# Kernel optimization log

Hardware: AMD Instinct MI355X
Metric: run time of the kernel (lower is better)

Reference implementation:

```python
import jax, jax.numpy as jnp
import numpy as np

DIM = 1024
CTX_DIM = 1024
VALUE_DIM = 1024
HEADS = 16
HEAD_DIM = DIM // HEADS        # q/k head dim = 64
V_HEAD_DIM = VALUE_DIM // HEADS
LN_EPS = 1e-5


def setup_inputs() -> dict:
    key = jax.random.key(0)
    k0, k1, k2, k3, k4 = jax.random.split(key, 5)
    B, N, M = 4, 1024, 1024
    x = jax.random.normal(k0, (B, N, DIM), jnp.float32)
    context = jax.random.normal(k1, (B, M, CTX_DIM), jnp.float32)
    # Linear weights stored as [in, out] (y = x @ W), matching torch Linear math
    Wq = jax.random.normal(k2, (DIM, DIM), jnp.float32) * (DIM ** -0.5)
    Wkv = jax.random.normal(k3, (CTX_DIM, DIM + VALUE_DIM), jnp.float32) * (CTX_DIM ** -0.5)
    Wt = jax.random.normal(k4, (HEADS, HEADS), jnp.float32) * (HEADS ** -0.5)
    gamma = jnp.ones((HEADS,), jnp.float32)
    beta = jnp.zeros((HEADS,), jnp.float32)
    return {"x": x, "context": context, "Wq": Wq, "Wkv": Wkv,
            "Wt": Wt, "gamma": gamma, "beta": beta}


def reference(x, context, Wq, Wkv, Wt, gamma, beta):
    B, N, _ = x.shape
    M = context.shape[1]
    # projections
    q = (x @ Wq).reshape(B, N, HEADS, HEAD_DIM).transpose(0, 2, 1, 3)       # [B,H,N,d]
    kv = context @ Wkv                                                      # [B,M,dim+vdim]
    k = kv[..., :DIM].reshape(B, M, HEADS, HEAD_DIM).transpose(0, 2, 1, 3)  # [B,H,M,d]
    v = kv[..., DIM:].reshape(B, M, HEADS, V_HEAD_DIM).transpose(0, 2, 1, 3)
    # scaled dot-product scores, fully materialized as in the original
    scale = HEAD_DIM ** -0.5
    dots = jnp.einsum('bhid,bhjd->bhij', q * scale, k)                      # [B,H,N,M]
    w = jax.nn.softmax(dots, axis=-1)
    # talking heads: Linear(heads,heads,bias=False) then LayerNorm(heads) over head axis
    w = jnp.einsum('bhij,hg->bgij', w, Wt)
    mu = jnp.mean(w, axis=1, keepdims=True)
    var = jnp.var(w, axis=1, keepdims=True)
    w = (w - mu) * jax.lax.rsqrt(var + LN_EPS)
    w = w * gamma[None, :, None, None] + beta[None, :, None, None]
    attn = jnp.einsum('bhij,bhjd->bhid', w, v)                              # [B,H,N,vd]
    out = attn.transpose(0, 2, 1, 3).reshape(B, N, VALUE_DIM)
    return out
```

## Files before the change

kernel.cpp:

```cpp
#include <hip/hip_runtime.h>
#include <hip/hip_bf16.h>

typedef __bf16 bf16;
typedef bf16 bf16x2 __attribute__((ext_vector_type(2)));
typedef bf16 bf16x4 __attribute__((ext_vector_type(4)));
typedef bf16 bf16x8 __attribute__((ext_vector_type(8)));
typedef float floatx4 __attribute__((ext_vector_type(4)));

#define MFMA_BF16(a, b, c) __builtin_amdgcn_mfma_f32_16x16x32_bf16((a), (b), (c), 0, 0, 0)

__global__ __launch_bounds__(256) void cvt_kernel(const float* __restrict__ in,
                                                  bf16* __restrict__ out, int n8) {
    int idx = blockIdx.x * 256 + threadIdx.x;
    if (idx >= n8) return;
    const float* src = in + (size_t)idx * 8;
    float4 f0 = *(const float4*)src;
    float4 f1 = *(const float4*)(src + 4);
    bf16x8 v = {(bf16)f0.x, (bf16)f0.y, (bf16)f0.z, (bf16)f0.w,
                (bf16)f1.x, (bf16)f1.y, (bf16)f1.z, (bf16)f1.w};
    *(bf16x8*)(out + (size_t)idx * 8) = v;
}

__global__ __launch_bounds__(256) void trans_kernel(const float* __restrict__ in,
                                                    bf16* __restrict__ out, int R, int C) {
    __shared__ float tile[32][33];
    const int t = threadIdx.x;
    const int r0 = blockIdx.y * 32, c0 = blockIdx.x * 32;
    int r = t >> 3, c4 = (t & 7) * 4;
    float4 v = *(const float4*)&in[(size_t)(r0 + r) * C + c0 + c4];
    tile[r][c4 + 0] = v.x; tile[r][c4 + 1] = v.y;
    tile[r][c4 + 2] = v.z; tile[r][c4 + 3] = v.w;
    __syncthreads();
    int rp = t >> 3, cp = (t & 7) * 4;
    bf16x4 w = {(bf16)tile[cp + 0][rp], (bf16)tile[cp + 1][rp],
                (bf16)tile[cp + 2][rp], (bf16)tile[cp + 3][rp]};
    *(bf16x4*)&out[(size_t)(c0 + rp) * R + r0 + cp] = w;
}

__global__ __launch_bounds__(256) void vtrans_kernel(const bf16* __restrict__ in,
                                                     bf16* __restrict__ out) {
    __shared__ bf16 tile[32][36];
    const int t = threadIdx.x;
    const int r0 = blockIdx.y * 32, c0 = blockIdx.x * 32;
    int r = t >> 3, c4 = (t & 7) * 4;
    bf16x4 v = *(const bf16x4*)&in[(size_t)(r0 + r) * 1024 + c0 + c4];
    tile[r][c4 + 0] = v[0]; tile[r][c4 + 1] = v[1];
    tile[r][c4 + 2] = v[2]; tile[r][c4 + 3] = v[3];
    __syncthreads();
    int rp = t >> 3, cp = (t & 7) * 4;
    int hd = c0 + rp;
    int b = r0 >> 10, j = (r0 & 1023) + cp;
    bf16x4 w = {tile[cp + 0][rp], tile[cp + 1][rp], tile[cp + 2][rp], tile[cp + 3][rp]};
    *(bf16x4*)&out[(size_t)(b * 1024 + hd) * 1024 + j] = w;
}

__global__ __launch_bounds__(256) void prep_wt_kernel(const float* __restrict__ Wt,
                                                      bf16* __restrict__ WtcT) {
    const int t = threadIdx.x;
    const int g = t >> 4, k = t & 15;
    float s = 0.f;
#pragma unroll
    for (int gg = 0; gg < 16; ++gg) s += Wt[k * 16 + gg];
    WtcT[g * 32 + k] = (bf16)(Wt[k * 16 + g] - s * 0.0625f);
    WtcT[g * 32 + 16 + k] = (bf16)0.f;
}

template <int MODE>
__global__ __launch_bounds__(256) void gemm128(const bf16* __restrict__ A,
                                               const bf16* __restrict__ B,
                                               bf16* __restrict__ C,
                                               bf16* __restrict__ V, int N) {
    __shared__ bf16 As[128 * 40];
    __shared__ bf16 Bs[128 * 40];
    const int t = threadIdx.x;
    const int wv = t >> 6, lane = t & 63, quad = lane >> 4, l15 = lane & 15;
    const int wr = wv >> 1, wc = wv & 1;
    const int m0 = blockIdx.y * 128, n0 = blockIdx.x * 128;
    const int ra = t >> 1, kc = (t & 1) * 16;

    floatx4 acc[4][4] = {};

    for (int k0 = 0; k0 < 1024; k0 += 32) {
        bf16x8 a0 = *(const bf16x8*)&A[(size_t)(m0 + ra) * 1024 + k0 + kc];
        bf16x8 a1 = *(const bf16x8*)&A[(size_t)(m0 + ra) * 1024 + k0 + kc + 8];
        bf16x8 b0 = *(const bf16x8*)&B[(size_t)(n0 + ra) * 1024 + k0 + kc];
        bf16x8 b1 = *(const bf16x8*)&B[(size_t)(n0 + ra) * 1024 + k0 + kc + 8];
        __syncthreads();
        *(bf16x8*)&As[ra * 40 + kc] = a0;
        *(bf16x8*)&As[ra * 40 + kc + 8] = a1;
        *(bf16x8*)&Bs[ra * 40 + kc] = b0;
        *(bf16x8*)&Bs[ra * 40 + kc + 8] = b1;
        __syncthreads();
        bf16x8 af[4], bfr[4];
#pragma unroll
        for (int mt = 0; mt < 4; ++mt)
            af[mt] = *(bf16x8*)&As[(wr * 64 + mt * 16 + l15) * 40 + quad * 8];
#pragma unroll
        for (int nt = 0; nt < 4; ++nt)
            bfr[nt] = *(bf16x8*)&Bs[(wc * 64 + nt * 16 + l15) * 40 + quad * 8];
#pragma unroll
        for (int mt = 0; mt < 4; ++mt)
#pragma unroll
            for (int nt = 0; nt < 4; ++nt)
                acc[mt][nt] = MFMA_BF16(af[mt], bfr[nt], acc[mt][nt]);
    }
#pragma unroll
    for (int mt = 0; mt < 4; ++mt)
#pragma unroll
        for (int nt = 0; nt < 4; ++nt)
#pragma unroll
            for (int r = 0; r < 4; ++r) {
                int m = m0 + wr * 64 + mt * 16 + quad * 4 + r;
                int n = n0 + wc * 64 + nt * 16 + l15;
                bf16 val = (bf16)acc[mt][nt][r];
                if (MODE == 0) {
                    C[(size_t)m * N + n] = val;
                } else {
                    if (n < 1024) C[(size_t)m * 1024 + n] = val;
                    else          V[(size_t)m * 1024 + (n - 1024)] = val;
                }
            }
}

__global__ __launch_bounds__(256, 4) void denom_kernel(const bf16* __restrict__ Qb,
                                                       const bf16* __restrict__ Kb,
                                                       float* __restrict__ L) {
    const int t = threadIdx.x;
    const int wv = t >> 6, lane = t & 63, quad = lane >> 4, l15 = lane & 15;
    unsigned n = blockIdx.x + (blockIdx.y << 5) + (blockIdx.z << 7);
    unsigned o = (n & 7) * 256 + (n >> 3);
    const int i0 = (o & 31) * 32;
    const int b  = (o >> 5) & 3;
    const int jz = o >> 7;
    const float scale = 0.125f;
    const bf16* Kbase = Kb + (size_t)b * 1024 * 1024;

    for (int hh = 0; hh < 4; ++hh) {
        const int h = wv * 4 + hh;
        bf16x8 qa[2][2];
#pragma unroll
        for (int it = 0; it < 2; ++it) {
            const bf16* qp = Qb + (size_t)(b * 1024 + i0 + it * 16 + l15) * 1024 +
                             h * 64 + quad * 8;
            qa[it][0] = *(const bf16x8*)qp;
            qa[it][1] = *(const bf16x8*)(qp + 32);
        }
        floatx4 se[2] = {};
#pragma unroll
        for (int jt = 0; jt < 4; ++jt) {
            int j = jz * 64 + jt * 16 + l15;
            const bf16* kp = Kbase + (size_t)j * 1024 + h * 64 + quad * 8;
            bf16x8 k0 = *(const bf16x8*)kp;
            bf16x8 k1 = *(const bf16x8*)(kp + 32);
#pragma unroll
            for (int it = 0; it < 2; ++it) {
                floatx4 c = {0.f, 0.f, 0.f, 0.f};
                c = MFMA_BF16(qa[it][0], k0, c);
                c = MFMA_BF16(qa[it][1], k1, c);
#pragma unroll
                for (int r = 0; r < 4; ++r) se[it][r] += __expf(c[r] * scale);
            }
        }
#pragma unroll
        for (int it = 0; it < 2; ++it)
#pragma unroll
            for (int r = 0; r < 4; ++r) {
                float s = se[it][r];
                s += __shfl_xor(s, 1); s += __shfl_xor(s, 2);
                s += __shfl_xor(s, 4); s += __shfl_xor(s, 8);
                if (l15 == 0)
                    atomicAdd(&L[(size_t)(b * 16 + h) * 1024 + i0 + it * 16 +
                                 quad * 4 + r], s);
            }
    }
}

__global__ __launch_bounds__(512, 4) void attn_kernel(const bf16* __restrict__ Qb,
                                                      const bf16* __restrict__ Kb,
                                                      const bf16* __restrict__ Vt,
                                                      const float* __restrict__ L,
                                                      const bf16* __restrict__ WtcT,
                                                      const float* __restrict__ gamma,
                                                      const float* __restrict__ beta,
                                                      float* __restrict__ out) {
    __shared__ bf16 Buf1[512 * 20];
    __shared__ bf16 Buf2[2 * 16 * 648];
    __shared__ __align__(16) bf16 Zbuf[8];
    const int t = threadIdx.x;
    const int wv = t >> 6, lane = t & 63, quad = lane >> 4, l15 = lane & 15;
    unsigned n = blockIdx.x + (blockIdx.y << 6) + (blockIdx.z << 8);
    unsigned o_idx = (n & 7) * 64 + (n >> 3);
    const int i0 = (o_idx & 63) * 16;
    const int b  = (o_idx >> 6) & 3;
    const int jz = o_idx >> 8;
    const float scale = 0.125f;

    if (t < 8) Zbuf[t] = (bf16)0.f;

    bf16x8 a_wt = *(const bf16x8*)&WtcT[l15 * 32 + quad * 8];
    float gq[4], bq[4];
#pragma unroll
    for (int r = 0; r < 4; ++r) { gq[r] = gamma[quad * 4 + r]; bq[r] = beta[quad * 4 + r]; }

    bf16x8 qa[2][2];
    float invl[2][4];
#pragma unroll
    for (int hh = 0; hh < 2; ++hh) {
        int h = wv * 2 + hh;
        const bf16* qp = Qb + (size_t)(b * 1024 + i0 + l15) * 1024 + h * 64 + quad * 8;
        qa[hh][0] = *(const bf16x8*)qp;
        qa[hh][1] = *(const bf16x8*)(qp + 32);
#pragma unroll
        for (int r = 0; r < 4; ++r)
            invl[hh][r] = 1.f / L[(size_t)(b * 16 + h) * 1024 + i0 + quad * 4 + r];
    }

    const bf16* Kbase = Kb + (size_t)b * 1024 * 1024;
    const bf16* Vbase = Vt + (size_t)b * 16 * 64 * 1024;
    floatx4 o[2][4] = {};

    auto S_phase = [&](int jt) {
        const int j0 = jz * 512 + jt * 32;
#pragma unroll
        for (int ns = 0; ns < 2; ++ns) {
            floatx4 cw[2];
#pragma unroll
            for (int hh = 0; hh < 2; ++hh) {
                int h = wv * 2 + hh;
                const bf16* kp = Kbase + (size_t)(j0 + ns * 16 + l15) * 1024 + h * 64 + quad * 8;
                floatx4 c = {0.f, 0.f, 0.f, 0.f};
                c = MFMA_BF16(qa[hh][0], *(const bf16x8*)kp, c);
                c = MFMA_BF16(qa[hh][1], *(const bf16x8*)(kp + 32), c);
                cw[hh] = c;
            }
#pragma unroll
            for (int r = 0; r < 4; ++r) {
                bf16x2 pk = {(bf16)(__expf(cw[0][r] * scale) * invl[0][r]),
                             (bf16)(__expf(cw[1][r] * scale) * invl[1][r])};
                *(bf16x2*)&Buf1[((quad * 4 + r) * 32 + ns * 16 + l15) * 20 + wv * 2] = pk;
            }
        }
    };
    auto PV = [&](int jtp) {
        const int j0 = jz * 512 + jtp * 32;
        const bf16* B2 = &Buf2[(jtp & 1) * 10368];
#pragma unroll
        for (int hh = 0; hh < 2; ++hh) {
            int g = wv * 2 + hh;
            bf16x8 a = *(const bf16x8*)&B2[g * 648 + l15 * 40 + quad * 8];
#pragma unroll
            for (int dt = 0; dt < 4; ++dt) {
                const bf16* vp = Vbase + (size_t)(g * 64 + dt * 16 + l15) * 1024 + j0 + quad * 8;
                o[hh][dt] = MFMA_BF16(a, *(const bf16x8*)vp, o[hh][dt]);
            }
        }
    };
    auto MIX = [&](int jt) {
        bf16* B2 = &Buf2[(jt & 1) * 10368];
#pragma unroll
        for (int grp = 0; grp < 4; ++grp) {
            int gi = wv * 4 + grp, ig = gi >> 1, jb = (gi & 1) * 16;
            int p = ig * 32 + jb + l15;
            const bf16* src = (quad < 2) ? &Buf1[p * 20 + quad * 8] : Zbuf;
            floatx4 c = {0.f, 0.f, 0.f, 0.f};
            c = MFMA_BF16(a_wt, *(const bf16x8*)src, c);
            float s2 = c[0] * c[0] + c[1] * c[1] + c[2] * c[2] + c[3] * c[3];
            s2 += __shfl_xor(s2, 16);
            s2 += __shfl_xor(s2, 32);
            float rs = rsqrtf(s2 * 0.0625f + 1e-5f);
#pragma unroll
            for (int r = 0; r < 4; ++r) {
                float w2 = c[r] * rs * gq[r] + bq[r];
                B2[(quad * 4 + r) * 648 + ig * 40 + jb + l15] = (bf16)w2;
            }
        }
    };

    S_phase(0);
    __syncthreads();
    MIX(0);
    __syncthreads();
    for (int jt = 1; jt < 16; ++jt) {
        S_phase(jt);
        PV(jt - 1);
        __syncthreads();
        MIX(jt);
        __syncthreads();
    }
    PV(15);

#pragma unroll
    for (int hh = 0; hh < 2; ++hh) {
        int g = wv * 2 + hh;
#pragma unroll
        for (int dt = 0; dt < 4; ++dt)
#pragma unroll
            for (int r = 0; r < 4; ++r)
                atomicAdd(&out[(size_t)(b * 1024 + i0 + quad * 4 + r) * 1024 +
                               g * 64 + dt * 16 + l15], o[hh][dt][r]);
    }
}

extern "C" void kernel_launch(void* const* d_in, const int* in_sizes, int n_in,
                              void* d_out, int out_size, void* d_ws, size_t ws_size,
                              hipStream_t stream) {
    const float* x     = (const float*)d_in[0];
    const float* ctx   = (const float*)d_in[1];
    const float* Wq    = (const float*)d_in[2];
    const float* Wkv   = (const float*)d_in[3];
    const float* Wt    = (const float*)d_in[4];
    const float* gamma = (const float*)d_in[5];
    const float* beta  = (const float*)d_in[6];
    float* out = (float*)d_out;

    bf16* xb   = (bf16*)d_ws;
    bf16* cb   = xb + (size_t)4 * 1024 * 1024;
    bf16* WqT  = cb + (size_t)4 * 1024 * 1024;
    bf16* WkvT = WqT + (size_t)1024 * 1024;
    bf16* Qb   = WkvT + (size_t)2048 * 1024;
    bf16* Kb   = Qb + (size_t)4 * 1024 * 1024;
    bf16* Vr   = Kb + (size_t)4 * 1024 * 1024;
    bf16* Vt   = Vr + (size_t)4 * 1024 * 1024;
    float* L   = (float*)(Vt + (size_t)4 * 1024 * 1024);
    bf16* WtcT = Vr;

    hipMemsetAsync(L, 0, (size_t)4 * 16 * 1024 * sizeof(float), stream);
    hipMemsetAsync(out, 0, (size_t)out_size * sizeof(float), stream);

    cvt_kernel<<<2048, 256, 0, stream>>>(x, xb, 524288);
    cvt_kernel<<<2048, 256, 0, stream>>>(ctx, cb, 524288);
    trans_kernel<<<dim3(32, 32), 256, 0, stream>>>(Wq, WqT, 1024, 1024);
    trans_kernel<<<dim3(64, 32), 256, 0, stream>>>(Wkv, WkvT, 1024, 2048);

    gemm128<0><<<dim3(8, 32), 256, 0, stream>>>(xb, WqT, Qb, nullptr, 1024);
    gemm128<1><<<dim3(16, 32), 256, 0, stream>>>(cb, WkvT, Kb, Vr, 2048);
    vtrans_kernel<<<dim3(32, 128), 256, 0, stream>>>(Vr, Vt);
    prep_wt_kernel<<<1, 256, 0, stream>>>(Wt, WtcT);

    denom_kernel<<<dim3(32, 4, 16), 256, 0, stream>>>(Qb, Kb, L);
    attn_kernel<<<dim3(64, 4, 2), 512, 0, stream>>>(Qb, Kb, Vt, L, WtcT, gamma, beta, out);
}
```

Measured before the change: 372.2 us.

## Double-buffer score tile and pipeline S, MIX, PV with one barrier per step

The single score buffer `Buf1` becomes double-buffered. The main loop is reorganised so that each iteration computes scores for tile jt, does PV for tile jt-2 and mixes tile jt-1, separated by one `__syncthreads` instead of two. The mixed-weight buffer drops its row padding (648 to 640) and adds a row-dependent 8-element offset to keep LDS bank conflicts low. The zero vector now lives in an unused slot of that buffer. The aim is to cut barrier stalls and overlap more work per step, at the cost of more LDS per block and an extra prologue and epilogue stage.

After: 369.5 us. About the same (-0.7%).

```diff
diff --git a/kernel.cpp b/kernel.cpp
--- a/kernel.cpp
+++ b/kernel.cpp
@@ -183,9 +183,8 @@
                                                       const float* __restrict__ gamma,
                                                       const float* __restrict__ beta,
                                                       float* __restrict__ out) {
-    __shared__ bf16 Buf1[512 * 20];
-    __shared__ bf16 Buf2[2 * 16 * 648];
-    __shared__ __align__(16) bf16 Zbuf[8];
+    __shared__ bf16 Buf1[2][512 * 20];
+    __shared__ bf16 Buf2[2][16 * 640];
     const int t = threadIdx.x;
     const int wv = t >> 6, lane = t & 63, quad = lane >> 4, l15 = lane & 15;
     unsigned n = blockIdx.x + (blockIdx.y << 6) + (blockIdx.z << 8);
@@ -195,7 +194,8 @@
     const int jz = o_idx >> 8;
     const float scale = 0.125f;
 
-    if (t < 8) Zbuf[t] = (bf16)0.f;
+    if (t < 8) Buf2[0][2560 + t] = (bf16)0.f;
+    const bf16* Zbuf = &Buf2[0][2560];
 
     bf16x8 a_wt = *(const bf16x8*)&WtcT[l15 * 32 + quad * 8];
     float gq[4], bq[4];
@@ -220,6 +220,7 @@
     floatx4 o[2][4] = {};
 
     auto S_phase = [&](int jt) {
+        bf16* B1 = Buf1[jt & 1];
         const int j0 = jz * 512 + jt * 32;
 #pragma unroll
         for (int ns = 0; ns < 2; ++ns) {
@@ -237,31 +238,18 @@
             for (int r = 0; r < 4; ++r) {
                 bf16x2 pk = {(bf16)(__expf(cw[0][r] * scale) * invl[0][r]),
                              (bf16)(__expf(cw[1][r] * scale) * invl[1][r])};
-                *(bf16x2*)&Buf1[((quad * 4 + r) * 32 + ns * 16 + l15) * 20 + wv * 2] = pk;
-            }
-        }
-    };
-    auto PV = [&](int jtp) {
-        const int j0 = jz * 512 + jtp * 32;
-        const bf16* B2 = &Buf2[(jtp & 1) * 10368];
-#pragma unroll
-        for (int hh = 0; hh < 2; ++hh) {
-            int g = wv * 2 + hh;
-            bf16x8 a = *(const bf16x8*)&B2[g * 648 + l15 * 40 + quad * 8];
-#pragma unroll
-            for (int dt = 0; dt < 4; ++dt) {
-                const bf16* vp = Vbase + (size_t)(g * 64 + dt * 16 + l15) * 1024 + j0 + quad * 8;
-                o[hh][dt] = MFMA_BF16(a, *(const bf16x8*)vp, o[hh][dt]);
+                *(bf16x2*)&B1[((quad * 4 + r) * 32 + ns * 16 + l15) * 20 + wv * 2] = pk;
             }
         }
     };
     auto MIX = [&](int jt) {
-        bf16* B2 = &Buf2[(jt & 1) * 10368];
+        const bf16* B1 = Buf1[jt & 1];
+        bf16* B2 = Buf2[jt & 1];
 #pragma unroll
         for (int grp = 0; grp < 4; ++grp) {
             int gi = wv * 4 + grp, ig = gi >> 1, jb = (gi & 1) * 16;
             int p = ig * 32 + jb + l15;
-            const bf16* src = (quad < 2) ? &Buf1[p * 20 + quad * 8] : Zbuf;
+            const bf16* src = (quad < 2) ? &B1[p * 20 + quad * 8] : Zbuf;
             floatx4 c = {0.f, 0.f, 0.f, 0.f};
             c = MFMA_BF16(a_wt, *(const bf16x8*)src, c);
             float s2 = c[0] * c[0] + c[1] * c[1] + c[2] * c[2] + c[3] * c[3];
@@ -271,22 +259,35 @@
 #pragma unroll
             for (int r = 0; r < 4; ++r) {
                 float w2 = c[r] * rs * gq[r] + bq[r];
-                B2[(quad * 4 + r) * 648 + ig * 40 + jb + l15] = (bf16)w2;
+                B2[(quad * 4 + r) * 640 + (quad & 1) * 8 + ig * 40 + jb + l15] = (bf16)w2;
             }
         }
     };
+    auto PV = [&](int jt) {
+        const bf16* B2 = Buf2[jt & 1];
+        const int j0 = jz * 512 + jt * 32;
+#pragma unroll
+        for (int hh = 0; hh < 2; ++hh) {
+            int g = wv * 2 + hh;
+            bf16x8 a = *(const bf16x8*)&B2[g * 640 + ((g >> 2) & 1) * 8 + l15 * 40 + quad * 8];
+#pragma unroll
+            for (int dt = 0; dt < 4; ++dt) {
+                const bf16* vp = Vbase + (size_t)(g * 64 + dt * 16 + l15) * 1024 + j0 + quad * 8;
+                o[hh][dt] = MFMA_BF16(a, *(const bf16x8*)vp, o[hh][dt]);
+            }
+        }
+    };
 
     S_phase(0);
     __syncthreads();
-    MIX(0);
-    __syncthreads();
-    for (int jt = 1; jt < 16; ++jt) {
-        S_phase(jt);
-        PV(jt - 1);
+    S_phase(1); MIX(0);
+    __syncthreads();
+    for (int jt = 2; jt < 16; ++jt) {
+        S_phase(jt); PV(jt - 2); MIX(jt - 1);
         __syncthreads();
-        MIX(jt);
-        __syncthreads();
-    }
+    }
+    PV(14); MIX(15);
+    __syncthreads();
     PV(15);
 
 #pragma unroll
```
